# Kernel optimization log

Measured on AMD Instinct MI355X. Metric: run time of the kernel, lower is better.

Reference implementation:

```python
import jax, jax.numpy as jnp
import numpy as np

B = 16384      # batch
IN = 512       # input width
G, F, O = 64, 24, 16      # hidden: groups, fan_in, group_out (width = G*O = 1024)
GO_G, GO_F, GO_O = 4, 48, 16  # output layer: 4 groups x 16 = 64 outputs


def setup_inputs() -> dict:
    key = jax.random.key(0)
    ks = jax.random.split(key, 13)
    # total columns available (concat of input + all prior hidden layers)
    tot = [IN, IN + G * O, IN + 2 * G * O, IN + 3 * G * O]  # 512,1536,2560,3584
    scale = 0.1
    return {
        "x": jax.random.normal(ks[0], (B, IN), jnp.float32),
        "W1": jax.random.normal(ks[1], (G, F, O), jnp.float32) * scale,
        "b1": jnp.zeros((G, O), jnp.float32),
        "W2": jax.random.normal(ks[2], (G, F, O), jnp.float32) * scale,
        "b2": jnp.zeros((G, O), jnp.float32),
        "W3": jax.random.normal(ks[3], (G, F, O), jnp.float32) * scale,
        "b3": jnp.zeros((G, O), jnp.float32),
        "Wo": jax.random.normal(ks[4], (GO_G, GO_F, GO_O), jnp.float32) * scale,
        "bo": jnp.zeros((GO_G, GO_O), jnp.float32),
        "idx1": jax.random.randint(ks[5], (G, F), 0, tot[0], jnp.int32),
        "idx2": jax.random.randint(ks[6], (G, F), 0, tot[1], jnp.int32),
        "idx3": jax.random.randint(ks[7], (G, F), 0, tot[2], jnp.int32),
        "idxo": jax.random.randint(ks[8], (GO_G, GO_F), 0, tot[3], jnp.int32),
    }


def _group_layer(acc, idx, W, b, act):
    # acc: [B, P] concat of all prior layer outputs; idx: [G, F] column coords
    g = acc[:, idx]                               # [B, G, F] irregular gather
    h = jnp.einsum('bgf,gfo->bgo', g, W) + b      # many tiny dense sublayers
    h = act(h)
    return h.reshape(h.shape[0], -1)              # concat groups -> [B, G*O]


def reference(x, W1, b1, W2, b2, W3, b3, Wo, bo, idx1, idx2, idx3, idxo):
    acc = x
    for idx, W, b in ((idx1, W1, b1), (idx2, W2, b2), (idx3, W3, b3)):
        out = _group_layer(acc, idx, W, b, jnp.tanh)
        acc = jnp.concatenate([acc, out], axis=1)  # inputs.append(layer_out)
    # output layer uses linear out_activation
    return _group_layer(acc, idxo, Wo, bo, lambda h: h)  # [B, 64]
```

## Files before the change

### kernel.cpp

```cpp
#include <hip/hip_runtime.h>
#include <hip/hip_bf16.h>


typedef unsigned short ushort_t;
typedef unsigned int uint_t;
typedef __attribute__((ext_vector_type(8))) short short8;
typedef __attribute__((ext_vector_type(4))) float f32x4;

#define ACC_STRIDE 3588
#define ROW_BYTES (ACC_STRIDE * 2)
#define PAD_ONE 3584
#define ONE_BYTE (PAD_ONE * 2)
#define ZERO_BYTE (3586 * 2)
#define ACC_U16 (16 * ACC_STRIDE)
#define OFFS_U16 6400
#define LDS_BYTES (ACC_U16 * 2 + OFFS_U16 * 2)

#define OFF_HIDO_B 204800
#define OFF_HEADO_B (204800 + 12288)

#define BF16_ONE ((short)0x3f80)

__device__ __forceinline__ ushort_t f2bf(float f) {
    __hip_bfloat16 h = __float2bfloat16(f);
    union { __hip_bfloat16 h; ushort_t u; } v;
    v.h = h;
    return v.u;
}

__device__ __forceinline__ uint_t pack2bf(float lo, float hi) {
    return (uint_t)f2bf(lo) | ((uint_t)f2bf(hi) << 16);
}

__device__ __forceinline__ float fast_tanh(float x) {
    float e = __expf(2.0f * x);
    return fmaf(-2.0f, __builtin_amdgcn_rcpf(e + 1.0f), 1.0f);
}

__device__ __forceinline__ void gather8(const char* accb, uint4 o, short8& af) {
    af[0] = *(const short*)(accb + (o.x & 0xffffu));
    af[1] = *(const short*)(accb + (o.x >> 16));
    af[2] = *(const short*)(accb + (o.y & 0xffffu));
    af[3] = *(const short*)(accb + (o.y >> 16));
    af[4] = *(const short*)(accb + (o.z & 0xffffu));
    af[5] = *(const short*)(accb + (o.z >> 16));
    af[6] = *(const short*)(accb + (o.w & 0xffffu));
    af[7] = *(const short*)(accb + (o.w >> 16));
}

__global__ __launch_bounds__(256)
void convert_weights(const float* __restrict__ W1, const float* __restrict__ b1,
                     const float* __restrict__ W2, const float* __restrict__ b2,
                     const float* __restrict__ W3, const float* __restrict__ b3,
                     const float* __restrict__ Wo, const float* __restrict__ bo,
                     const int* __restrict__ idx1, const int* __restrict__ idx2,
                     const int* __restrict__ idx3, const int* __restrict__ idxo,
                     ushort_t* __restrict__ ws)
{
    const int tid = blockIdx.x * 256 + threadIdx.x;
    const int lane = tid & 63;
    const int nn = lane & 15;
    const int quad = lane >> 4;
    if (tid < 12288) {
        const int g = (tid >> 6) & 63;
        const int l = tid >> 12;
        const float* W = (l == 0) ? W1 : (l == 1) ? W2 : W3;
        const float* bb = (l == 0) ? b1 : (l == 1) ? b2 : b3;
        const float* Wg = W + g * 384;
        ushort_t v[8];
        #pragma unroll
        for (int j = 0; j < 8; ++j) {
            const int k = quad * 8 + j;
            v[j] = (k < 24) ? f2bf(Wg[k * 16 + nn])
                 : (k == 24) ? f2bf(bb[g * 16 + nn]) : (ushort_t)0;
        }
        ushort4* dst = reinterpret_cast<ushort4*>(ws + (size_t)tid * 8);
        dst[0] = make_ushort4(v[0], v[1], v[2], v[3]);
        dst[1] = make_ushort4(v[4], v[5], v[6], v[7]);
    } else if (tid < 12800) {
        const int h = tid - 12288;
        const int gs = h >> 6;
        const int go = gs >> 1;
        const int step = gs & 1;
        const float* Wg = Wo + go * 768;
        ushort_t v[8];
        #pragma unroll
        for (int j = 0; j < 8; ++j) {
            const int k = step * 32 + quad * 8 + j;
            v[j] = (k < 48) ? f2bf(Wg[k * 16 + nn])
                 : (k == 48) ? f2bf(bo[go * 16 + nn]) : (ushort_t)0;
        }
        ushort4* dst = reinterpret_cast<ushort4*>(ws + (size_t)tid * 8);
        dst[0] = make_ushort4(v[0], v[1], v[2], v[3]);
        dst[1] = make_ushort4(v[4], v[5], v[6], v[7]);
    } else if (tid < 18944) {
        const int e = tid - 12800;
        const int l = e >> 11;
        const int rem = e & 2047;
        const int g = rem >> 5;
        const int k = rem & 31;
        const int* idx = (l == 0) ? idx1 : (l == 1) ? idx2 : idx3;
        const int v = (k < 24) ? idx[g * 24 + k] * 2
                    : (k == 24) ? ONE_BYTE : ZERO_BYTE;
        reinterpret_cast<ushort_t*>((char*)ws + OFF_HIDO_B)[e] = (ushort_t)v;
    } else if (tid < 19200) {
        const int e = tid - 18944;
        const int go = e >> 6;
        const int k = e & 63;
        const int v = (k < 48) ? idxo[go * 48 + k] * 2
                    : (k == 48) ? ONE_BYTE : ZERO_BYTE;
        reinterpret_cast<ushort_t*>((char*)ws + OFF_HEADO_B)[e] = (ushort_t)v;
    }
}

#define NTILES 4

__global__ __launch_bounds__(1024)
void demodel_mfma(const float* __restrict__ x,
                  const ushort_t* __restrict__ ws,
                  float* __restrict__ out)
{
    extern __shared__ __align__(16) ushort_t smem[];
    const int t = threadIdx.x;
    const int lane = t & 63;
    const int wv = t >> 6;
    const int nn = lane & 15;
    const int quad = lane >> 4;

    {
        const uint4* src = reinterpret_cast<const uint4*>((const char*)ws + OFF_HIDO_B);
        uint4* dst = reinterpret_cast<uint4*>(smem + ACC_U16);
        for (int i = t; i < (OFFS_U16 * 2) / 16; i += 1024)
            dst[i] = src[i];
    }

    const ushort_t* offsu = smem + ACC_U16;
    const char* accb = (const char*)smem + nn * ROW_BYTES;
    char* accw = (char*)smem;

    const int pr = (t - 512) >> 5;
    const int pc = (t & 31) << 4;
    uint_t px[8];

    if (wv >= 8) {
        const float4* src = reinterpret_cast<const float4*>(
            x + ((size_t)blockIdx.x * 16 + pr) * 512 + pc);
        float4 a0 = src[0], a1 = src[1], a2 = src[2], a3 = src[3];
        px[0] = pack2bf(a0.x, a0.y); px[1] = pack2bf(a0.z, a0.w);
        px[2] = pack2bf(a1.x, a1.y); px[3] = pack2bf(a1.z, a1.w);
        px[4] = pack2bf(a2.x, a2.y); px[5] = pack2bf(a2.z, a2.w);
        px[6] = pack2bf(a3.x, a3.y); px[7] = pack2bf(a3.z, a3.w);
    }

    #pragma unroll 1
    for (int it = 0; it < NTILES; ++it) {
        const int row0 = (it * 256 + blockIdx.x) * 16;

        __syncthreads();
        if (wv >= 8) {
            uint2* d = reinterpret_cast<uint2*>(accw + pr * ROW_BYTES + pc * 2);
            d[0] = make_uint2(px[0], px[1]);
            d[1] = make_uint2(px[2], px[3]);
            d[2] = make_uint2(px[4], px[5]);
            d[3] = make_uint2(px[6], px[7]);
        }
        __syncthreads();

        #pragma unroll 1
        for (int l = 0; l < 3; ++l) {
            const int out_base = 512 + l * 1024;
            const int g0 = wv << 2;

            short8 bfr[4];
            #pragma unroll
            for (int gi = 0; gi < 4; ++gi)
                bfr[gi] = *reinterpret_cast<const short8*>(
                    ws + (((size_t)l * 64 + g0 + gi) * 64 + lane) * 8);

            short8 af[4];
            if (quad < 3) {
                uint4 ofs[4];
                #pragma unroll
                for (int gi = 0; gi < 4; ++gi)
                    ofs[gi] = *reinterpret_cast<const uint4*>(
                        offsu + l * 2048 + (g0 + gi) * 32 + quad * 8);
                #pragma unroll
                for (int gi = 0; gi < 4; ++gi)
                    gather8(accb, ofs[gi], af[gi]);
            } else {
                #pragma unroll
                for (int gi = 0; gi < 4; ++gi) {
                    short8 c = {};
                    c[0] = BF16_ONE;
                    af[gi] = c;
                }
            }

            f32x4 acc[4];
            #pragma unroll
            for (int gi = 0; gi < 4; ++gi) {
                f32x4 z = { 0.f, 0.f, 0.f, 0.f };
                acc[gi] = __builtin_amdgcn_mfma_f32_16x16x32_bf16(bfr[gi], af[gi], z, 0, 0, 0);
            }

            #pragma unroll
            for (int gi = 0; gi < 4; ++gi) {
                const int colo = out_base + (g0 + gi) * 16 + quad * 4;
                uint2 w = make_uint2(
                    pack2bf(fast_tanh(acc[gi][0]), fast_tanh(acc[gi][1])),
                    pack2bf(fast_tanh(acc[gi][2]), fast_tanh(acc[gi][3])));
                *reinterpret_cast<uint2*>(accw + nn * ROW_BYTES + colo * 2) = w;
            }
            __syncthreads();
        }

        if (wv < 4) {
            const int go = wv;
            short8 bfr0 = *reinterpret_cast<const short8*>(
                ws + (12288 + ((size_t)go * 2 + 0) * 64 + lane) * 8);
            short8 bfr1 = *reinterpret_cast<const short8*>(
                ws + (12288 + ((size_t)go * 2 + 1) * 64 + lane) * 8);

            short8 af0;
            {
                uint4 o = *reinterpret_cast<const uint4*>(
                    offsu + 6144 + go * 64 + quad * 8);
                gather8(accb, o, af0);
            }
            short8 af1;
            if (quad < 2) {
                uint4 o = *reinterpret_cast<const uint4*>(
                    offsu + 6144 + go * 64 + 32 + quad * 8);
                gather8(accb, o, af1);
            } else {
                short8 c = {};
                if (quad == 2) c[0] = BF16_ONE;
                af1 = c;
            }

            f32x4 z = { 0.f, 0.f, 0.f, 0.f };
            f32x4 a0 = __builtin_amdgcn_mfma_f32_16x16x32_bf16(bfr0, af0, z, 0, 0, 0);
            f32x4 a1 = __builtin_amdgcn_mfma_f32_16x16x32_bf16(bfr1, af1, z, 0, 0, 0);
            float4 o;
            o.x = a0[0] + a1[0];
            o.y = a0[1] + a1[1];
            o.z = a0[2] + a1[2];
            o.w = a0[3] + a1[3];
            *reinterpret_cast<float4*>(
                out + (size_t)(row0 + nn) * 64 + go * 16 + quad * 4) = o;
        }
        if (wv >= 8 && it + 1 < NTILES) {
            const float4* src = reinterpret_cast<const float4*>(
                x + (((size_t)(it + 1) * 256 + blockIdx.x) * 16 + pr) * 512 + pc);
            float4 a0 = src[0], a1 = src[1], a2 = src[2], a3 = src[3];
            px[0] = pack2bf(a0.x, a0.y); px[1] = pack2bf(a0.z, a0.w);
            px[2] = pack2bf(a1.x, a1.y); px[3] = pack2bf(a1.z, a1.w);
            px[4] = pack2bf(a2.x, a2.y); px[5] = pack2bf(a2.z, a2.w);
            px[6] = pack2bf(a3.x, a3.y); px[7] = pack2bf(a3.z, a3.w);
        }
    }
}

extern "C" void kernel_launch(void* const* d_in, const int* in_sizes, int n_in,
                              void* d_out, int out_size, void* d_ws, size_t ws_size,
                              hipStream_t stream) {
    const float* x  = (const float*)d_in[0];
    const float* W1 = (const float*)d_in[1];
    const float* b1 = (const float*)d_in[2];
    const float* W2 = (const float*)d_in[3];
    const float* b2 = (const float*)d_in[4];
    const float* W3 = (const float*)d_in[5];
    const float* b3 = (const float*)d_in[6];
    const float* Wo = (const float*)d_in[7];
    const float* bo = (const float*)d_in[8];
    const int* idx1 = (const int*)d_in[9];
    const int* idx2 = (const int*)d_in[10];
    const int* idx3 = (const int*)d_in[11];
    const int* idxo = (const int*)d_in[12];
    float* out = (float*)d_out;

    (void)hipFuncSetAttribute((const void*)demodel_mfma,
                              hipFuncAttributeMaxDynamicSharedMemorySize,
                              LDS_BYTES);

    convert_weights<<<75, 256, 0, stream>>>(W1, b1, W2, b2, W3, b3, Wo, bo,
                                            idx1, idx2, idx3, idxo,
                                            (ushort_t*)d_ws);

    demodel_mfma<<<256, 1024, LDS_BYTES, stream>>>(
        x, (const ushort_t*)d_ws, out);
}
```

Before: 121.9 us.

## Double-buffer the input tile in LDS to drop a per-tile barrier

```diff
diff --git a/kernel.cpp b/kernel.cpp
--- a/kernel.cpp
+++ b/kernel.cpp
@@ -7,17 +7,14 @@
 typedef __attribute__((ext_vector_type(8))) short short8;
 typedef __attribute__((ext_vector_type(4))) float f32x4;
 
-#define ACC_STRIDE 3588
+#define ACC_STRIDE 4102
 #define ROW_BYTES (ACC_STRIDE * 2)
-#define PAD_ONE 3584
-#define ONE_BYTE (PAD_ONE * 2)
-#define ZERO_BYTE (3586 * 2)
+#define HID_BASE 1024
 #define ACC_U16 (16 * ACC_STRIDE)
-#define OFFS_U16 6400
+#define OFFS_U16 12800
 #define LDS_BYTES (ACC_U16 * 2 + OFFS_U16 * 2)
 
 #define OFF_HIDO_B 204800
-#define OFF_HEADO_B (204800 + 12288)
 
 #define BF16_ONE ((short)0x3f80)
 
@@ -93,23 +90,27 @@
         ushort4* dst = reinterpret_cast<ushort4*>(ws + (size_t)tid * 8);
         dst[0] = make_ushort4(v[0], v[1], v[2], v[3]);
         dst[1] = make_ushort4(v[4], v[5], v[6], v[7]);
-    } else if (tid < 18944) {
+    } else if (tid < 25600) {
         const int e = tid - 12800;
-        const int l = e >> 11;
-        const int rem = e & 2047;
-        const int g = rem >> 5;
-        const int k = rem & 31;
-        const int* idx = (l == 0) ? idx1 : (l == 1) ? idx2 : idx3;
-        const int v = (k < 24) ? idx[g * 24 + k] * 2
-                    : (k == 24) ? ONE_BYTE : ZERO_BYTE;
+        const int p = (e >= 6400) ? 1 : 0;
+        const int r = e - p * 6400;
+        int c = -1;
+        if (r < 6144) {
+            const int l = r >> 11;
+            const int rem = r & 2047;
+            const int g = rem >> 5;
+            const int k = rem & 31;
+            const int* idx = (l == 0) ? idx1 : (l == 1) ? idx2 : idx3;
+            if (k < 24) c = idx[g * 24 + k];
+        } else {
+            const int r2 = r - 6144;
+            const int go = r2 >> 6;
+            const int k = r2 & 63;
+            if (k < 48) c = idxo[go * 48 + k];
+        }
+        const int v = (c < 0) ? 0
+                    : ((c < 512) ? (p * 512 + c) * 2 : (c + 512) * 2);
         reinterpret_cast<ushort_t*>((char*)ws + OFF_HIDO_B)[e] = (ushort_t)v;
-    } else if (tid < 19200) {
-        const int e = tid - 18944;
-        const int go = e >> 6;
-        const int k = e & 63;
-        const int v = (k < 48) ? idxo[go * 48 + k] * 2
-                    : (k == 48) ? ONE_BYTE : ZERO_BYTE;
-        reinterpret_cast<ushort_t*>((char*)ws + OFF_HEADO_B)[e] = (ushort_t)v;
     }
 }
 
@@ -150,25 +151,23 @@
         px[2] = pack2bf(a1.x, a1.y); px[3] = pack2bf(a1.z, a1.w);
         px[4] = pack2bf(a2.x, a2.y); px[5] = pack2bf(a2.z, a2.w);
         px[6] = pack2bf(a3.x, a3.y); px[7] = pack2bf(a3.z, a3.w);
-    }
+        uint2* d = reinterpret_cast<uint2*>(accw + pr * ROW_BYTES + pc * 2);
+        d[0] = make_uint2(px[0], px[1]);
+        d[1] = make_uint2(px[2], px[3]);
+        d[2] = make_uint2(px[4], px[5]);
+        d[3] = make_uint2(px[6], px[7]);
+    }
+    __syncthreads();
 
     #pragma unroll 1
     for (int it = 0; it < NTILES; ++it) {
         const int row0 = (it * 256 + blockIdx.x) * 16;
-
-        __syncthreads();
-        if (wv >= 8) {
-            uint2* d = reinterpret_cast<uint2*>(accw + pr * ROW_BYTES + pc * 2);
-            d[0] = make_uint2(px[0], px[1]);
-            d[1] = make_uint2(px[2], px[3]);
-            d[2] = make_uint2(px[4], px[5]);
-            d[3] = make_uint2(px[6], px[7]);
-        }
-        __syncthreads();
+        const int p = it & 1;
+        const ushort_t* tb = offsu + p * 6400;
 
         #pragma unroll 1
         for (int l = 0; l < 3; ++l) {
-            const int out_base = 512 + l * 1024;
+            const int out_base = HID_BASE + l * 1024;
             const int g0 = wv << 2;
 
             short8 bfr[4];
@@ -183,7 +182,7 @@
                 #pragma unroll
                 for (int gi = 0; gi < 4; ++gi)
                     ofs[gi] = *reinterpret_cast<const uint4*>(
-                        offsu + l * 2048 + (g0 + gi) * 32 + quad * 8);
+                        tb + l * 2048 + (g0 + gi) * 32 + quad * 8);
                 #pragma unroll
                 for (int gi = 0; gi < 4; ++gi)
                     gather8(accb, ofs[gi], af[gi]);
@@ -224,13 +223,13 @@
             short8 af0;
             {
                 uint4 o = *reinterpret_cast<const uint4*>(
-                    offsu + 6144 + go * 64 + quad * 8);
+                    tb + 6144 + go * 64 + quad * 8);
                 gather8(accb, o, af0);
             }
             short8 af1;
             if (quad < 2) {
                 uint4 o = *reinterpret_cast<const uint4*>(
-                    offsu + 6144 + go * 64 + 32 + quad * 8);
+                    tb + 6144 + go * 64 + 32 + quad * 8);
                 gather8(accb, o, af1);
             } else {
                 short8 c = {};
@@ -257,7 +256,15 @@
             px[2] = pack2bf(a1.x, a1.y); px[3] = pack2bf(a1.z, a1.w);
             px[4] = pack2bf(a2.x, a2.y); px[5] = pack2bf(a2.z, a2.w);
             px[6] = pack2bf(a3.x, a3.y); px[7] = pack2bf(a3.z, a3.w);
-        }
+            const int xb = (p ^ 1) * 512;
+            uint2* d = reinterpret_cast<uint2*>(
+                accw + pr * ROW_BYTES + (xb + pc) * 2);
+            d[0] = make_uint2(px[0], px[1]);
+            d[1] = make_uint2(px[2], px[3]);
+            d[2] = make_uint2(px[4], px[5]);
+            d[3] = make_uint2(px[6], px[7]);
+        }
+        __syncthreads();
     }
 }
 
@@ -283,9 +290,9 @@
                               hipFuncAttributeMaxDynamicSharedMemorySize,
                               LDS_BYTES);
 
-    convert_weights<<<75, 256, 0, stream>>>(W1, b1, W2, b2, W3, b3, Wo, bo,
-                                            idx1, idx2, idx3, idxo,
-                                            (ushort_t*)d_ws);
+    convert_weights<<<100, 256, 0, stream>>>(W1, b1, W2, b2, W3, b3, Wo, bo,
+                                             idx1, idx2, idx3, idxo,
+                                             (ushort_t*)d_ws);
 
     demodel_mfma<<<256, 1024, LDS_BYTES, stream>>>(
         x, (const ushort_t*)d_ws, out);
```

Result: slower. 135.1 us (+10.8%).
